# Kernel tuning notes

Measured on AMD Instinct MI355X. Metric: run time of the kernel, lower is better.

Reference implementation:

```python
import jax, jax.numpy as jnp
import numpy as np

EMBED = 1024
HEADS = 16
HEAD_DIM = EMBED // HEADS
HIDDEN = 4 * EMBED
EPS = 1e-6


def setup_inputs() -> dict:
    key = jax.random.key(0)
    ks = jax.random.split(key, 8)
    s = 0.02
    return {
        "x": jax.random.normal(ks[0], (2, 2048, EMBED), dtype=jnp.float32),
        "ln1_w": jnp.ones((EMBED,), jnp.float32),
        "ln1_b": jnp.zeros((EMBED,), jnp.float32),
        "qkv_w": jax.random.normal(ks[1], (3 * EMBED, EMBED), jnp.float32) * s,
        "qkv_b": jnp.zeros((3 * EMBED,), jnp.float32),
        "proj_w": jax.random.normal(ks[2], (EMBED, EMBED), jnp.float32) * s,
        "proj_b": jnp.zeros((EMBED,), jnp.float32),
        "ln2_w": jnp.ones((EMBED,), jnp.float32),
        "ln2_b": jnp.zeros((EMBED,), jnp.float32),
        "fc1_w": jax.random.normal(ks[3], (HIDDEN, EMBED), jnp.float32) * s,
        "fc1_b": jnp.zeros((HIDDEN,), jnp.float32),
        "fc2_w": jax.random.normal(ks[4], (EMBED, HIDDEN), jnp.float32) * s,
        "fc2_b": jnp.zeros((EMBED,), jnp.float32),
    }


def _layernorm(x, w, b):
    mu = jnp.mean(x, axis=-1, keepdims=True)
    var = jnp.mean(jnp.square(x - mu), axis=-1, keepdims=True)
    return (x - mu) * jax.lax.rsqrt(var + EPS) * w + b


def _attn(x, qkv_w, qkv_b, proj_w, proj_b):
    B, S, E = x.shape
    qkv = x @ qkv_w.T + qkv_b                      # [B,S,3E]
    qkv = qkv.reshape(B, S, 3, HEADS, HEAD_DIM)
    q, k, v = jnp.moveaxis(qkv, 2, 0)              # each [B,S,H,D]
    q = q.transpose(0, 2, 1, 3)                    # [B,H,S,D]
    k = k.transpose(0, 2, 1, 3)
    v = v.transpose(0, 2, 1, 3)
    scale = HEAD_DIM ** -0.5
    scores = jnp.einsum("bhqd,bhkd->bhqk", q, k) * scale
    mask = jnp.tril(jnp.ones((S, S), dtype=bool))
    scores = jnp.where(mask, scores, -jnp.inf)
    attn = jax.nn.softmax(scores, axis=-1)
    out = jnp.einsum("bhqk,bhkd->bhqd", attn, v)   # [B,H,S,D]
    out = out.transpose(0, 2, 1, 3).reshape(B, S, E)
    return out @ proj_w.T + proj_b


def reference(x, ln1_w, ln1_b, qkv_w, qkv_b, proj_w, proj_b,
              ln2_w, ln2_b, fc1_w, fc1_b, fc2_w, fc2_b):
    x = x + _attn(_layernorm(x, ln1_w, ln1_b), qkv_w, qkv_b, proj_w, proj_b)
    h = _layernorm(x, ln2_w, ln2_b)
    h = jax.nn.gelu(h @ fc1_w.T + fc1_b, approximate=False)
    x = x + (h @ fc2_w.T + fc2_b)
    return x
```

## Files before the change

### kernel.cpp

```cpp
#include <hip/hip_runtime.h>
#include <hip/hip_bf16.h>


#define E_    1024
#define TE_   3072
#define S_    2048
#define B_    2
#define H_    16
#define MROWS 4096

typedef __attribute__((ext_vector_type(8))) short bf16x8;
typedef __attribute__((ext_vector_type(4))) short short4v;
typedef __attribute__((ext_vector_type(4))) float f32x4;

__device__ __forceinline__ short f2bf(float f) {
  union { float f; unsigned u; } v; v.f = f;
  unsigned r = v.u + 0x7fffu + ((v.u >> 16) & 1u);
  return (short)(r >> 16);
}
__device__ __forceinline__ float bf2f(short s) {
  union { unsigned u; float f; } v; v.u = ((unsigned)(unsigned short)s) << 16;
  return v.f;
}
__device__ __forceinline__ void gload_lds16(const void* g, void* l) {
  __builtin_amdgcn_global_load_lds(
      (const __attribute__((address_space(1))) unsigned int*)g,
      (__attribute__((address_space(3))) unsigned int*)l, 16, 0, 0);
}
__device__ __forceinline__ float exp2_fast(float x) {
  float r; asm("v_exp_f32 %0, %1" : "=v"(r) : "v"(x)); return r;
}
__device__ __forceinline__ float gelu_f(float v) {
  return 0.5f * v * (1.0f + erff(v * 0.70710678118654752f));
}

__global__ __launch_bounds__(256) void k_cvt4(const float* __restrict__ i0, short* __restrict__ o0, int n0,
                                              const float* __restrict__ i1, short* __restrict__ o1, int n1,
                                              const float* __restrict__ i2, short* __restrict__ o2, int n2,
                                              const float* __restrict__ i3, short* __restrict__ o3, int n3) {
  const float* in; short* out; int n;
  switch (blockIdx.y) {
    case 0: in = i0; out = o0; n = n0; break;
    case 1: in = i1; out = o1; n = n1; break;
    case 2: in = i2; out = o2; n = n2; break;
    default: in = i3; out = o3; n = n3; break;
  }
  int i = blockIdx.x * 256 + threadIdx.x;
  if (i >= n) return;
  float4 v = ((const float4*)in)[i];
  short4v o = { f2bf(v.x), f2bf(v.y), f2bf(v.z), f2bf(v.w) };
  ((short4v*)out)[i] = o;
}

__global__ __launch_bounds__(256) void k_ln(const float* __restrict__ x,
                                            const float* __restrict__ w,
                                            const float* __restrict__ b,
                                            short* __restrict__ out) {
  int row = blockIdx.x;
  int tid = threadIdx.x;
  float4 v = ((const float4*)(x + (size_t)row * E_))[tid];
  float s  = v.x + v.y + v.z + v.w;
  float s2 = v.x*v.x + v.y*v.y + v.z*v.z + v.w*v.w;
  #pragma unroll
  for (int d = 1; d < 64; d <<= 1) { s += __shfl_xor(s, d); s2 += __shfl_xor(s2, d); }
  __shared__ float rs[4], rq[4];
  int wv = tid >> 6;
  if ((tid & 63) == 0) { rs[wv] = s; rq[wv] = s2; }
  __syncthreads();
  s  = rs[0] + rs[1] + rs[2] + rs[3];
  s2 = rq[0] + rq[1] + rq[2] + rq[3];
  float mu  = s * (1.0f / E_);
  float var = fmaxf(s2 * (1.0f / E_) - mu * mu, 0.0f);
  float inv = rsqrtf(var + 1e-6f);
  float4 wv4 = ((const float4*)w)[tid];
  float4 bv4 = ((const float4*)b)[tid];
  short4v o = { f2bf((v.x - mu) * inv * wv4.x + bv4.x),
                f2bf((v.y - mu) * inv * wv4.y + bv4.y),
                f2bf((v.z - mu) * inv * wv4.z + bv4.z),
                f2bf((v.w - mu) * inv * wv4.w + bv4.w) };
  ((short4v*)(out + (size_t)row * E_))[tid] = o;
}

template <int EPI>
__global__ __launch_bounds__(256, 3) void k_gemm(const short* __restrict__ A,
                                                 const short* __restrict__ W,
                                                 const float* __restrict__ bias,
                                                 const float* __restrict__ res,
                                                 void* __restrict__ outv,
                                                 int M, int N, int K) {
  __shared__ short As[2][128 * 32];
  __shared__ short Ws[2][128 * 32];
  int tid  = threadIdx.x;
  int lane = tid & 63, wave = tid >> 6;
  int wm = wave >> 1, wn = wave & 1;
  int m0 = blockIdx.y * 128, n0 = blockIdx.x * 128;
  int fr = lane & 15, fq = lane >> 4, fk = fq * 8;

  f32x4 acc[4][4];
  #pragma unroll
  for (int i = 0; i < 4; ++i)
    #pragma unroll
    for (int j = 0; j < 4; ++j) acc[i][j] = (f32x4){0.f, 0.f, 0.f, 0.f};

  int sr = tid >> 2;
  int sc = (tid & 3) * 8;
  const short* Arow  = A + (size_t)(m0 + sr) * K + sc;
  const short* Wrow  = W + (size_t)(n0 + sr) * K + sc;
  const short* Arow2 = A + (size_t)(m0 + 64 + sr) * K + sc;
  const short* Wrow2 = W + (size_t)(n0 + 64 + sr) * K + sc;

#define STAGE_(buf, k0)                                   \
  do {                                                    \
    gload_lds16(Arow  + (k0), &As[buf][tid * 8]);         \
    gload_lds16(Arow2 + (k0), &As[buf][2048 + tid * 8]);  \
    gload_lds16(Wrow  + (k0), &Ws[buf][tid * 8]);         \
    gload_lds16(Wrow2 + (k0), &Ws[buf][2048 + tid * 8]);  \
  } while (0)

#define COMPUTE_(buf)                                                         \
  do {                                                                        \
    bf16x8 af[4], bfr[4];                                                     \
    _Pragma("unroll")                                                         \
    for (int i = 0; i < 4; ++i) {                                             \
      af[i]  = *(const bf16x8*)(&As[buf][(wm * 64 + i * 16 + fr) * 32 + fk]); \
      bfr[i] = *(const bf16x8*)(&Ws[buf][(wn * 64 + i * 16 + fr) * 32 + fk]); \
    }                                                                         \
    _Pragma("unroll")                                                         \
    for (int mi = 0; mi < 4; ++mi)                                            \
      _Pragma("unroll")                                                       \
      for (int ni = 0; ni < 4; ++ni)                                          \
        acc[mi][ni] = __builtin_amdgcn_mfma_f32_16x16x32_bf16(                \
            af[mi], bfr[ni], acc[mi][ni], 0, 0, 0);                           \
  } while (0)

  int nt = K >> 5;
  STAGE_(0, 0);
  __syncthreads();
  int cur = 0;
  for (int t = 0; t < nt - 1; ++t) {
    STAGE_(cur ^ 1, (t + 1) * 32);
    COMPUTE_(cur);
    __syncthreads();
    cur ^= 1;
  }
  COMPUTE_(cur);

#undef STAGE_
#undef COMPUTE_

  #pragma unroll
  for (int mi = 0; mi < 4; ++mi) {
    #pragma unroll
    for (int ni = 0; ni < 4; ++ni) {
      int gm0 = m0 + wm * 64 + mi * 16 + fq * 4;
      int gn  = n0 + wn * 64 + ni * 16 + fr;
      float bv = bias[gn];
      #pragma unroll
      for (int j = 0; j < 4; ++j) {
        size_t idx = (size_t)(gm0 + j) * N + gn;
        float v = acc[mi][ni][j] + bv;
        if (EPI == 0)      ((short*)outv)[idx] = f2bf(v);
        else if (EPI == 1) ((float*)outv)[idx] = v + res[idx];
        else               ((short*)outv)[idx] = f2bf(gelu_f(v));
      }
    }
  }
}

__global__ __launch_bounds__(256) void k_attn(const short* __restrict__ qkv,
                                              short* __restrict__ out) {
  __shared__ short Kt[64 * 64];
  __shared__ short Vt[64 * 64];
  __shared__ short Pl[4][1024];
  int tid  = threadIdx.x;
  int lane = tid & 63, w = tid >> 6;
  int qb   = (int)gridDim.x - 1 - (int)blockIdx.x;
  int q0   = qb * 64;
  int bh   = blockIdx.y;
  int b    = bh >> 4, h = bh & 15;
  int fr   = lane & 15, fq = lane >> 4, fk = fq * 8;
  const float sc = 0.18033688011112042f;

  const short* qp = qkv + (size_t)(b * S_ + q0 + w * 16 + fr) * TE_ + h * 64;
  bf16x8 qa0 = *(const bf16x8*)(qp + fk);
  bf16x8 qa1 = *(const bf16x8*)(qp + 32 + fk);

  float m_r = -__builtin_inff();
  float l_r = 0.f;
  f32x4 o[4];
  #pragma unroll
  for (int c = 0; c < 4; ++c) o[c] = (f32x4){0.f, 0.f, 0.f, 0.f};

  int srow = tid >> 3;
  int schunk = tid & 7;
  short* Pw = &Pl[w][0];

  for (int kv = 0; kv <= q0; kv += 64) {
    __syncthreads();
    #pragma unroll
    for (int r = 0; r < 2; ++r) {
      int row = srow + 32 * r;
      size_t grow = (size_t)(b * S_ + kv + row) * TE_ + h * 64;
      gload_lds16(qkv + grow + E_ + ((schunk ^ (srow & 7)) << 3),
                  Kt + r * 2048 + tid * 8);
      bf16x8 vv = *(const bf16x8*)(qkv + grow + 2 * E_ + (schunk << 3));
      int kc = row >> 3, kwi = row & 7;
      #pragma unroll
      for (int j = 0; j < 8; ++j) {
        int d = (schunk << 3) + j;
        int csw = kc ^ (d & 7) ^ ((d >> 3) & 7);
        Vt[d * 64 + csw * 8 + kwi] = vv[j];
      }
    }
    __syncthreads();

    f32x4 s[4];
    #pragma unroll
    for (int g = 0; g < 4; ++g) {
      const short* kb = Kt + ((g << 4) + fr) * 64;
      int sw = fr & 7;
      bf16x8 a0 = *(const bf16x8*)(kb + ((fq ^ sw) << 3));
      bf16x8 a1 = *(const bf16x8*)(kb + (((4 + fq) ^ sw) << 3));
      f32x4 t = (f32x4){0.f, 0.f, 0.f, 0.f};
      t = __builtin_amdgcn_mfma_f32_16x16x32_bf16(a0, qa0, t, 0, 0, 0);
      t = __builtin_amdgcn_mfma_f32_16x16x32_bf16(a1, qa1, t, 0, 0, 0);
      s[g] = t;
    }
    #pragma unroll
    for (int g = 0; g < 4; ++g)
      #pragma unroll
      for (int jj = 0; jj < 4; ++jj) s[g][jj] *= sc;

    if (kv + 64 > q0) {
      int qr = (q0 - kv) + 16 * w + fr;
      #pragma unroll
      for (int g = 0; g < 4; ++g)
        #pragma unroll
        for (int jj = 0; jj < 4; ++jj)
          if (16 * g + 4 * fq + jj > qr) s[g][jj] = -__builtin_inff();
    }

    float mg0 = fmaxf(fmaxf(s[0][0], s[0][1]), fmaxf(s[0][2], s[0][3]));
    float mg1 = fmaxf(fmaxf(s[1][0], s[1][1]), fmaxf(s[1][2], s[1][3]));
    float mg2 = fmaxf(fmaxf(s[2][0], s[2][1]), fmaxf(s[2][2], s[2][3]));
    float mg3 = fmaxf(fmaxf(s[3][0], s[3][1]), fmaxf(s[3][2], s[3][3]));
    float mt = fmaxf(fmaxf(mg0, mg1), fmaxf(mg2, mg3));
    mt = fmaxf(mt, __shfl_xor(mt, 16));
    mt = fmaxf(mt, __shfl_xor(mt, 32));
    float mn = fmaxf(m_r, mt);
    float al = exp2_fast(m_r - mn);
    m_r = mn;
    #pragma unroll
    for (int g = 0; g < 4; ++g)
      #pragma unroll
      for (int jj = 0; jj < 4; ++jj) s[g][jj] = exp2_fast(s[g][jj] - mn);
    f32x4 s4 = s[0] + s[1] + s[2] + s[3];
    float ps = (s4[0] + s4[1]) + (s4[2] + s4[3]);
    ps += __shfl_xor(ps, 16);
    ps += __shfl_xor(ps, 32);
    l_r = l_r * al + ps;

    #pragma unroll
    for (int g = 0; g < 4; ++g) {
      short4v pk = { f2bf(s[g][0]), f2bf(s[g][1]), f2bf(s[g][2]), f2bf(s[g][3]) };
      int pc = (2 * g + (fq >> 1)) ^ (fr & 7);
      *(short4v*)(Pw + fr * 64 + pc * 8 + ((fq & 1) << 2)) = pk;
    }

    #pragma unroll
    for (int c = 0; c < 4; ++c)
      #pragma unroll
      for (int jj = 0; jj < 4; ++jj) o[c][jj] *= al;

    bf16x8 pb0 = *(const bf16x8*)(Pw + fr * 64 + ((fq ^ (fr & 7)) << 3));
    bf16x8 pb1 = *(const bf16x8*)(Pw + fr * 64 + (((4 + fq) ^ (fr & 7)) << 3));
    #pragma unroll
    for (int c = 0; c < 4; ++c) {
      int d = 16 * c + fr;
      int sbase = (d & 7) ^ ((d >> 3) & 7);
      const short* vb = Vt + d * 64;
      bf16x8 va0 = *(const bf16x8*)(vb + ((fq ^ sbase) << 3));
      bf16x8 va1 = *(const bf16x8*)(vb + (((4 + fq) ^ sbase) << 3));
      o[c] = __builtin_amdgcn_mfma_f32_16x16x32_bf16(va0, pb0, o[c], 0, 0, 0);
      o[c] = __builtin_amdgcn_mfma_f32_16x16x32_bf16(va1, pb1, o[c], 0, 0, 0);
    }
  }

  float inv_l = 1.0f / l_r;
  #pragma unroll
  for (int c = 0; c < 4; ++c) {
    short4v okk = { f2bf(o[c][0] * inv_l), f2bf(o[c][1] * inv_l),
                    f2bf(o[c][2] * inv_l), f2bf(o[c][3] * inv_l) };
    int pc = (2 * c + (fq >> 1)) ^ (fr & 7);
    *(short4v*)(Pw + fr * 64 + pc * 8 + ((fq & 1) << 2)) = okk;
  }
  int ql = lane >> 2, dc = lane & 3;
  int swz = ql & 7;
  const short* ob = Pw + ql * 64;
  bf16x8 r0 = *(const bf16x8*)(ob + (((2 * dc) ^ swz) << 3));
  bf16x8 r1 = *(const bf16x8*)(ob + (((2 * dc + 1) ^ swz) << 3));
  short* op = out + (size_t)(b * S_ + q0 + 16 * w + ql) * E_ + h * 64 + dc * 16;
  *(bf16x8*)op = r0;
  *(bf16x8*)(op + 8) = r1;
}

extern "C" void kernel_launch(void* const* d_in, const int* in_sizes, int n_in,
                              void* d_out, int out_size, void* d_ws, size_t ws_size,
                              hipStream_t stream) {
  const float* x      = (const float*)d_in[0];
  const float* ln1_w  = (const float*)d_in[1];
  const float* ln1_b  = (const float*)d_in[2];
  const float* qkv_w  = (const float*)d_in[3];
  const float* qkv_b  = (const float*)d_in[4];
  const float* proj_w = (const float*)d_in[5];
  const float* proj_b = (const float*)d_in[6];
  const float* ln2_w  = (const float*)d_in[7];
  const float* ln2_b  = (const float*)d_in[8];
  const float* fc1_w  = (const float*)d_in[9];
  const float* fc1_b  = (const float*)d_in[10];
  const float* fc2_w  = (const float*)d_in[11];
  const float* fc2_b  = (const float*)d_in[12];
  float* out = (float*)d_out;

  char* ws = (char*)d_ws;
  short* xn1    = (short*)(ws + 0);
  short* qkvb   = (short*)(ws + (8u  << 20));
  short* gelu_o = (short*)(ws + 0);
  short* attn_o = (short*)(ws + (32u << 20));
  short* h_ln2  = (short*)(ws + (32u << 20));
  float* x_res  = (float*)(ws + (40u << 20));
  short* w_qkv  = (short*)(ws + (56u << 20));
  short* w_proj = (short*)(ws + (62u << 20));
  short* w_fc1  = (short*)(ws + (64u << 20));
  short* w_fc2  = (short*)(ws + (72u << 20));

  k_cvt4<<<dim3(4096, 4), 256, 0, stream>>>(qkv_w, w_qkv, 786432,
                                            proj_w, w_proj, 262144,
                                            fc1_w, w_fc1, 1048576,
                                            fc2_w, w_fc2, 1048576);

  k_ln<<<MROWS, 256, 0, stream>>>(x, ln1_w, ln1_b, xn1);
  k_gemm<0><<<dim3(24, 32), 256, 0, stream>>>(xn1, w_qkv, qkv_b, nullptr, qkvb,
                                              MROWS, TE_, E_);
  k_attn<<<dim3(S_ / 64, B_ * H_), 256, 0, stream>>>(qkvb, attn_o);
  k_gemm<1><<<dim3(8, 32), 256, 0, stream>>>(attn_o, w_proj, proj_b, x, x_res,
                                             MROWS, E_, E_);
  k_ln<<<MROWS, 256, 0, stream>>>(x_res, ln2_w, ln2_b, h_ln2);
  k_gemm<2><<<dim3(32, 32), 256, 0, stream>>>(h_ln2, w_fc1, fc1_b, nullptr, gelu_o,
                                              MROWS, 4096, E_);
  k_gemm<1><<<dim3(8, 32), 256, 0, stream>>>(gelu_o, w_fc2, fc2_b, x_res, out,
                                             MROWS, E_, 4096);
}
```

Before: 413.9 us.

## Double-buffer K/V tiles and process 128 query rows per attention block

The attention kernel now handles 128 query rows per block, with each wave owning two 16-row groups, so every K/V tile loaded into LDS is reused by twice as many queries. K and V tiles are double-buffered: the next tile's global loads are issued before the current tile's compute, which removes one barrier per iteration and overlaps memory latency with MFMA work. The cost is more registers and LDS per block (launch bounds ask for 3 blocks per CU), half as many blocks, and more wasted masked work on the diagonal tiles of the causal mask.

```diff
diff --git a/kernel.cpp b/kernel.cpp
--- a/kernel.cpp
+++ b/kernel.cpp
@@ -167,141 +167,209 @@
   }
 }
 
-__global__ __launch_bounds__(256) void k_attn(const short* __restrict__ qkv,
-                                              short* __restrict__ out) {
-  __shared__ short Kt[64 * 64];
-  __shared__ short Vt[64 * 64];
-  __shared__ short Pl[4][1024];
+__global__ __launch_bounds__(256, 3) void k_attn(const short* __restrict__ qkv,
+                                                 short* __restrict__ out) {
+  __shared__ short Kt[2][64 * 64];
+  __shared__ short Vt[2][64 * 64];
+  __shared__ short Pl[4][2048];
   int tid  = threadIdx.x;
   int lane = tid & 63, w = tid >> 6;
   int qb   = (int)gridDim.x - 1 - (int)blockIdx.x;
-  int q0   = qb * 64;
+  int q0   = qb * 128;
   int bh   = blockIdx.y;
   int b    = bh >> 4, h = bh & 15;
   int fr   = lane & 15, fq = lane >> 4, fk = fq * 8;
   const float sc = 0.18033688011112042f;
 
-  const short* qp = qkv + (size_t)(b * S_ + q0 + w * 16 + fr) * TE_ + h * 64;
-  bf16x8 qa0 = *(const bf16x8*)(qp + fk);
-  bf16x8 qa1 = *(const bf16x8*)(qp + 32 + fk);
-
-  float m_r = -__builtin_inff();
-  float l_r = 0.f;
-  f32x4 o[4];
-  #pragma unroll
-  for (int c = 0; c < 4; ++c) o[c] = (f32x4){0.f, 0.f, 0.f, 0.f};
+  bf16x8 qa[2][2];
+  #pragma unroll
+  for (int g2 = 0; g2 < 2; ++g2) {
+    const short* qp = qkv + (size_t)(b * S_ + q0 + w * 32 + g2 * 16 + fr) * TE_ + h * 64;
+    qa[g2][0] = *(const bf16x8*)(qp + fk);
+    qa[g2][1] = *(const bf16x8*)(qp + 32 + fk);
+  }
+
+  float m_r[2] = {-__builtin_inff(), -__builtin_inff()};
+  float l_r[2] = {0.f, 0.f};
+  f32x4 o[2][4];
+  #pragma unroll
+  for (int g2 = 0; g2 < 2; ++g2)
+    #pragma unroll
+    for (int c = 0; c < 4; ++c) o[g2][c] = (f32x4){0.f, 0.f, 0.f, 0.f};
 
   int srow = tid >> 3;
   int schunk = tid & 7;
   short* Pw = &Pl[w][0];
-
-  for (int kv = 0; kv <= q0; kv += 64) {
-    __syncthreads();
-    #pragma unroll
-    for (int r = 0; r < 2; ++r) {
-      int row = srow + 32 * r;
-      size_t grow = (size_t)(b * S_ + kv + row) * TE_ + h * 64;
-      gload_lds16(qkv + grow + E_ + ((schunk ^ (srow & 7)) << 3),
-                  Kt + r * 2048 + tid * 8);
-      bf16x8 vv = *(const bf16x8*)(qkv + grow + 2 * E_ + (schunk << 3));
-      int kc = row >> 3, kwi = row & 7;
-      #pragma unroll
-      for (int j = 0; j < 8; ++j) {
-        int d = (schunk << 3) + j;
-        int csw = kc ^ (d & 7) ^ ((d >> 3) & 7);
-        Vt[d * 64 + csw * 8 + kwi] = vv[j];
+  bf16x8 vv[2];
+
+#define V_LOAD_(kvv)                                                          \
+  do {                                                                        \
+    _Pragma("unroll")                                                         \
+    for (int r = 0; r < 2; ++r) {                                             \
+      size_t grow = (size_t)(b * S_ + (kvv) + srow + 32 * r) * TE_ + h * 64;  \
+      vv[r] = *(const bf16x8*)(qkv + grow + 2 * E_ + (schunk << 3));          \
+    }                                                                         \
+  } while (0)
+
+#define K_STAGE_(buf, kvv)                                                    \
+  do {                                                                        \
+    _Pragma("unroll")                                                         \
+    for (int r = 0; r < 2; ++r) {                                             \
+      size_t grow = (size_t)(b * S_ + (kvv) + srow + 32 * r) * TE_ + h * 64;  \
+      gload_lds16(qkv + grow + E_ + ((schunk ^ (srow & 7)) << 3),             \
+                  &Kt[buf][r * 2048 + tid * 8]);                              \
+    }                                                                         \
+  } while (0)
+
+#define V_WRITE_(buf)                                                         \
+  do {                                                                        \
+    _Pragma("unroll")                                                         \
+    for (int r = 0; r < 2; ++r) {                                             \
+      int row = srow + 32 * r;                                                \
+      int kc = row >> 3, kwi = row & 7;                                       \
+      _Pragma("unroll")                                                       \
+      for (int j = 0; j < 8; ++j) {                                           \
+        int d = (schunk << 3) + j;                                            \
+        int csw = kc ^ (d & 7) ^ ((d >> 3) & 7);                              \
+        Vt[buf][d * 64 + csw * 8 + kwi] = vv[r][j];                           \
+      }                                                                       \
+    }                                                                         \
+  } while (0)
+
+  V_LOAD_(0);
+  K_STAGE_(0, 0);
+  V_WRITE_(0);
+  __syncthreads();
+  int cur = 0;
+  int nt = 2 * qb + 2;
+
+  for (int t = 0; t < nt; ++t) {
+    int kv = t * 64;
+    if (t + 1 < nt) {
+      V_LOAD_((t + 1) * 64);
+      K_STAGE_(cur ^ 1, (t + 1) * 64);
+    }
+
+    int sw = fr & 7;
+    bf16x8 ka[4][2];
+    #pragma unroll
+    for (int g = 0; g < 4; ++g) {
+      const short* kb = &Kt[cur][((g << 4) + fr) * 64];
+      ka[g][0] = *(const bf16x8*)(kb + ((fq ^ sw) << 3));
+      ka[g][1] = *(const bf16x8*)(kb + (((4 + fq) ^ sw) << 3));
+    }
+    f32x4 s[2][4];
+    #pragma unroll
+    for (int g2 = 0; g2 < 2; ++g2)
+      #pragma unroll
+      for (int g = 0; g < 4; ++g) {
+        f32x4 t0 = (f32x4){0.f, 0.f, 0.f, 0.f};
+        t0 = __builtin_amdgcn_mfma_f32_16x16x32_bf16(ka[g][0], qa[g2][0], t0, 0, 0, 0);
+        t0 = __builtin_amdgcn_mfma_f32_16x16x32_bf16(ka[g][1], qa[g2][1], t0, 0, 0, 0);
+        s[g2][g] = t0;
       }
-    }
-    __syncthreads();
-
-    f32x4 s[4];
-    #pragma unroll
-    for (int g = 0; g < 4; ++g) {
-      const short* kb = Kt + ((g << 4) + fr) * 64;
-      int sw = fr & 7;
-      bf16x8 a0 = *(const bf16x8*)(kb + ((fq ^ sw) << 3));
-      bf16x8 a1 = *(const bf16x8*)(kb + (((4 + fq) ^ sw) << 3));
-      f32x4 t = (f32x4){0.f, 0.f, 0.f, 0.f};
-      t = __builtin_amdgcn_mfma_f32_16x16x32_bf16(a0, qa0, t, 0, 0, 0);
-      t = __builtin_amdgcn_mfma_f32_16x16x32_bf16(a1, qa1, t, 0, 0, 0);
-      s[g] = t;
-    }
-    #pragma unroll
-    for (int g = 0; g < 4; ++g)
-      #pragma unroll
-      for (int jj = 0; jj < 4; ++jj) s[g][jj] *= sc;
-
-    if (kv + 64 > q0) {
-      int qr = (q0 - kv) + 16 * w + fr;
+    #pragma unroll
+    for (int g2 = 0; g2 < 2; ++g2)
       #pragma unroll
       for (int g = 0; g < 4; ++g)
         #pragma unroll
-        for (int jj = 0; jj < 4; ++jj)
-          if (16 * g + 4 * fq + jj > qr) s[g][jj] = -__builtin_inff();
-    }
-
-    float mg0 = fmaxf(fmaxf(s[0][0], s[0][1]), fmaxf(s[0][2], s[0][3]));
-    float mg1 = fmaxf(fmaxf(s[1][0], s[1][1]), fmaxf(s[1][2], s[1][3]));
-    float mg2 = fmaxf(fmaxf(s[2][0], s[2][1]), fmaxf(s[2][2], s[2][3]));
-    float mg3 = fmaxf(fmaxf(s[3][0], s[3][1]), fmaxf(s[3][2], s[3][3]));
-    float mt = fmaxf(fmaxf(mg0, mg1), fmaxf(mg2, mg3));
-    mt = fmaxf(mt, __shfl_xor(mt, 16));
-    mt = fmaxf(mt, __shfl_xor(mt, 32));
-    float mn = fmaxf(m_r, mt);
-    float al = exp2_fast(m_r - mn);
-    m_r = mn;
-    #pragma unroll
-    for (int g = 0; g < 4; ++g)
-      #pragma unroll
-      for (int jj = 0; jj < 4; ++jj) s[g][jj] = exp2_fast(s[g][jj] - mn);
-    f32x4 s4 = s[0] + s[1] + s[2] + s[3];
-    float ps = (s4[0] + s4[1]) + (s4[2] + s4[3]);
-    ps += __shfl_xor(ps, 16);
-    ps += __shfl_xor(ps, 32);
-    l_r = l_r * al + ps;
-
-    #pragma unroll
-    for (int g = 0; g < 4; ++g) {
-      short4v pk = { f2bf(s[g][0]), f2bf(s[g][1]), f2bf(s[g][2]), f2bf(s[g][3]) };
-      int pc = (2 * g + (fq >> 1)) ^ (fr & 7);
-      *(short4v*)(Pw + fr * 64 + pc * 8 + ((fq & 1) << 2)) = pk;
-    }
-
-    #pragma unroll
-    for (int c = 0; c < 4; ++c)
-      #pragma unroll
-      for (int jj = 0; jj < 4; ++jj) o[c][jj] *= al;
-
-    bf16x8 pb0 = *(const bf16x8*)(Pw + fr * 64 + ((fq ^ (fr & 7)) << 3));
-    bf16x8 pb1 = *(const bf16x8*)(Pw + fr * 64 + (((4 + fq) ^ (fr & 7)) << 3));
+        for (int jj = 0; jj < 4; ++jj) s[g2][g][jj] *= sc;
+
+    if (kv + 64 > q0) {
+      #pragma unroll
+      for (int g2 = 0; g2 < 2; ++g2) {
+        int qr = (q0 - kv) + 32 * w + 16 * g2 + fr;
+        #pragma unroll
+        for (int g = 0; g < 4; ++g)
+          #pragma unroll
+          for (int jj = 0; jj < 4; ++jj)
+            if (16 * g + 4 * fq + jj > qr) s[g2][g][jj] = -__builtin_inff();
+      }
+    }
+
+    #pragma unroll
+    for (int g2 = 0; g2 < 2; ++g2) {
+      float mg0 = fmaxf(fmaxf(s[g2][0][0], s[g2][0][1]), fmaxf(s[g2][0][2], s[g2][0][3]));
+      float mg1 = fmaxf(fmaxf(s[g2][1][0], s[g2][1][1]), fmaxf(s[g2][1][2], s[g2][1][3]));
+      float mg2 = fmaxf(fmaxf(s[g2][2][0], s[g2][2][1]), fmaxf(s[g2][2][2], s[g2][2][3]));
+      float mg3 = fmaxf(fmaxf(s[g2][3][0], s[g2][3][1]), fmaxf(s[g2][3][2], s[g2][3][3]));
+      float mt = fmaxf(fmaxf(mg0, mg1), fmaxf(mg2, mg3));
+      mt = fmaxf(mt, __shfl_xor(mt, 16));
+      mt = fmaxf(mt, __shfl_xor(mt, 32));
+      float mn = fmaxf(m_r[g2], mt);
+      float al = exp2_fast(m_r[g2] - mn);
+      m_r[g2] = mn;
+      #pragma unroll
+      for (int g = 0; g < 4; ++g)
+        #pragma unroll
+        for (int jj = 0; jj < 4; ++jj) s[g2][g][jj] = exp2_fast(s[g2][g][jj] - mn);
+      f32x4 s4 = s[g2][0] + s[g2][1] + s[g2][2] + s[g2][3];
+      float ps = (s4[0] + s4[1]) + (s4[2] + s4[3]);
+      ps += __shfl_xor(ps, 16);
+      ps += __shfl_xor(ps, 32);
+      l_r[g2] = l_r[g2] * al + ps;
+
+      #pragma unroll
+      for (int g = 0; g < 4; ++g) {
+        short4v pk = { f2bf(s[g2][g][0]), f2bf(s[g2][g][1]),
+                       f2bf(s[g2][g][2]), f2bf(s[g2][g][3]) };
+        int pc = (2 * g + (fq >> 1)) ^ (fr & 7);
+        *(short4v*)(Pw + g2 * 1024 + fr * 64 + pc * 8 + ((fq & 1) << 2)) = pk;
+      }
+      #pragma unroll
+      for (int c = 0; c < 4; ++c)
+        #pragma unroll
+        for (int jj = 0; jj < 4; ++jj) o[g2][c][jj] *= al;
+    }
+
+    bf16x8 pb[2][2];
+    #pragma unroll
+    for (int g2 = 0; g2 < 2; ++g2) {
+      pb[g2][0] = *(const bf16x8*)(Pw + g2 * 1024 + fr * 64 + ((fq ^ (fr & 7)) << 3));
+      pb[g2][1] = *(const bf16x8*)(Pw + g2 * 1024 + fr * 64 + (((4 + fq) ^ (fr & 7)) << 3));
+    }
     #pragma unroll
     for (int c = 0; c < 4; ++c) {
       int d = 16 * c + fr;
       int sbase = (d & 7) ^ ((d >> 3) & 7);
-      const short* vb = Vt + d * 64;
+      const short* vb = &Vt[cur][d * 64];
       bf16x8 va0 = *(const bf16x8*)(vb + ((fq ^ sbase) << 3));
       bf16x8 va1 = *(const bf16x8*)(vb + (((4 + fq) ^ sbase) << 3));
-      o[c] = __builtin_amdgcn_mfma_f32_16x16x32_bf16(va0, pb0, o[c], 0, 0, 0);
-      o[c] = __builtin_amdgcn_mfma_f32_16x16x32_bf16(va1, pb1, o[c], 0, 0, 0);
-    }
-  }
-
-  float inv_l = 1.0f / l_r;
-  #pragma unroll
-  for (int c = 0; c < 4; ++c) {
-    short4v okk = { f2bf(o[c][0] * inv_l), f2bf(o[c][1] * inv_l),
-                    f2bf(o[c][2] * inv_l), f2bf(o[c][3] * inv_l) };
-    int pc = (2 * c + (fq >> 1)) ^ (fr & 7);
-    *(short4v*)(Pw + fr * 64 + pc * 8 + ((fq & 1) << 2)) = okk;
-  }
+      #pragma unroll
+      for (int g2 = 0; g2 < 2; ++g2) {
+        o[g2][c] = __builtin_amdgcn_mfma_f32_16x16x32_bf16(va0, pb[g2][0], o[g2][c], 0, 0, 0);
+        o[g2][c] = __builtin_amdgcn_mfma_f32_16x16x32_bf16(va1, pb[g2][1], o[g2][c], 0, 0, 0);
+      }
+    }
+
+    if (t + 1 < nt) V_WRITE_(cur ^ 1);
+    __syncthreads();
+    cur ^= 1;
+  }
+
+#undef V_LOAD_
+#undef K_STAGE_
+#undef V_WRITE_
+
   int ql = lane >> 2, dc = lane & 3;
   int swz = ql & 7;
-  const short* ob = Pw + ql * 64;
-  bf16x8 r0 = *(const bf16x8*)(ob + (((2 * dc) ^ swz) << 3));
-  bf16x8 r1 = *(const bf16x8*)(ob + (((2 * dc + 1) ^ swz) << 3));
-  short* op = out + (size_t)(b * S_ + q0 + 16 * w + ql) * E_ + h * 64 + dc * 16;
-  *(bf16x8*)op = r0;
-  *(bf16x8*)(op + 8) = r1;
+  #pragma unroll
+  for (int g2 = 0; g2 < 2; ++g2) {
+    float inv_l = 1.0f / l_r[g2];
+    #pragma unroll
+    for (int c = 0; c < 4; ++c) {
+      short4v okk = { f2bf(o[g2][c][0] * inv_l), f2bf(o[g2][c][1] * inv_l),
+                      f2bf(o[g2][c][2] * inv_l), f2bf(o[g2][c][3] * inv_l) };
+      int pc = (2 * c + (fq >> 1)) ^ (fr & 7);
+      *(short4v*)(Pw + g2 * 1024 + fr * 64 + pc * 8 + ((fq & 1) << 2)) = okk;
+    }
+    const short* ob = Pw + g2 * 1024 + ql * 64;
+    bf16x8 r0 = *(const bf16x8*)(ob + (((2 * dc) ^ swz) << 3));
+    bf16x8 r1 = *(const bf16x8*)(ob + (((2 * dc + 1) ^ swz) << 3));
+    short* op = out + (size_t)(b * S_ + q0 + 32 * w + 16 * g2 + ql) * E_ + h * 64 + dc * 16;
+    *(bf16x8*)op = r0;
+    *(bf16x8*)(op + 8) = r1;
+  }
 }
 
 extern "C" void kernel_launch(void* const* d_in, const int* in_sizes, int n_in,
@@ -342,7 +410,7 @@
   k_ln<<<MROWS, 256, 0, stream>>>(x, ln1_w, ln1_b, xn1);
   k_gemm<0><<<dim3(24, 32), 256, 0, stream>>>(xn1, w_qkv, qkv_b, nullptr, qkvb,
                                               MROWS, TE_, E_);
-  k_attn<<<dim3(S_ / 64, B_ * H_), 256, 0, stream>>>(qkvb, attn_o);
+  k_attn<<<dim3(S_ / 128, B_ * H_), 256, 0, stream>>>(qkvb, attn_o);
   k_gemm<1><<<dim3(8, 32), 256, 0, stream>>>(attn_o, w_proj, proj_b, x, x_res,
                                              MROWS, E_, E_);
   k_ln<<<MROWS, 256, 0, stream>>>(x_res, ln2_w, ln2_b, h_ln2);
```

After: 396.4 us. 4.2% less time.
